# Kernel tuning notes

Measured on AMD Instinct MI355X. Metric: run time of the kernel, lower is better.

## Reference

```python
import jax, jax.numpy as jnp
import numpy as np

N_OBJECTS = 30
N_POINTS = 500
BATCH = 16384
ROT_WEIGHT = 1.0
TRANS_WEIGHT = 1.0


def quat_to_mat(q):
    # q: [B,4] (w,x,y,z) -> [B,3,3]; matches the module's (unnormalized) formula
    w, x, y, z = q[:, 0], q[:, 1], q[:, 2], q[:, 3]
    x2, y2, z2 = x * x, y * y, z * z
    xy, xz, yz = x * y, x * z, y * z
    wx, wy, wz = w * x, w * y, w * z
    row0 = jnp.stack([1 - 2 * y2 - 2 * z2, 2 * xy - 2 * wz, 2 * xz + 2 * wy], axis=1)
    row1 = jnp.stack([2 * xy + 2 * wz, 1 - 2 * x2 - 2 * z2, 2 * yz - 2 * wx], axis=1)
    row2 = jnp.stack([2 * xz - 2 * wy, 2 * yz + 2 * wx, 1 - 2 * x2 - 2 * y2], axis=1)
    return jnp.stack([row0, row1, row2], axis=1)


def setup_inputs() -> dict:
    key = jax.random.key(0)
    k1, k2, k3, k4, k5, k6 = jax.random.split(key, 6)
    pred_r = jax.random.normal(k1, (BATCH, 4), dtype=jnp.float32)
    pred_t = jax.random.normal(k2, (BATCH, 3), dtype=jnp.float32)
    gt_r = jax.random.normal(k3, (BATCH, 4), dtype=jnp.float32)
    gt_t = jax.random.normal(k4, (BATCH, 3), dtype=jnp.float32)
    obj_ids = jax.random.randint(k5, (BATCH,), 0, N_OBJECTS, dtype=jnp.int64)
    # sampled 3D model points per object (stand-in for loaded .ply meshes, in meters)
    points = jax.random.normal(k6, (N_OBJECTS, N_POINTS, 3), dtype=jnp.float32) * 0.1
    return {"pred_r": pred_r, "pred_t": pred_t, "gt_r": gt_r, "gt_t": gt_t,
            "obj_ids": obj_ids, "points": points}


def reference(pred_r, pred_t, gt_r, gt_t, obj_ids, points):
    Rp = quat_to_mat(pred_r)  # [B,3,3]
    Rg = quat_to_mat(gt_r)
    pts = points[obj_ids]  # [B,N,3] gather per-sample model points
    # pts @ R^T for both rotations; the difference is all that's needed for ADD/rot
    rot_diff = jnp.einsum('bij,bnj->bni', Rp - Rg, pts)  # [B,N,3]
    t_diff = pred_t - gt_t  # [B,3]
    add = jnp.linalg.norm(rot_diff + t_diff[:, None, :], axis=-1).mean(axis=1)  # [B]
    rot = jnp.linalg.norm(rot_diff, axis=-1).mean(axis=1)  # [B]
    trans = jnp.linalg.norm(t_diff, axis=-1)  # [B]
    return add.mean() + ROT_WEIGHT * rot.mean() + TRANS_WEIGHT * trans.mean()
```

## Files before the change

### kernel.cpp

```cpp
#include <hip/hip_runtime.h>

#define BATCH 16384
#define NPTS  500
#define NOBJ  30
#define EPW   2
#define WPB   4
#define NBLK  (BATCH / (EPW * WPB))

typedef float v2f __attribute__((ext_vector_type(2)));

__device__ __forceinline__ float fsqrt(float x) {
    return __builtin_amdgcn_sqrtf(x);
}

__global__ __launch_bounds__(256) void add_loss_stage1(
    const float* __restrict__ pred_r,
    const float* __restrict__ pred_t,
    const float* __restrict__ gt_r,
    const float* __restrict__ gt_t,
    const int*   __restrict__ obj_ids,
    const float* __restrict__ points,
    float* __restrict__ partial)
{
    const int wave  = threadIdx.x >> 6;
    const int lane  = threadIdx.x & 63;
    const int gwave = blockIdx.x * WPB + wave;
    const int b0    = gwave * EPW;

    float acc_pts   = 0.0f;
    float acc_trans = 0.0f;

    #pragma unroll
    for (int e = 0; e < EPW; ++e) {
        const int b = b0 + e;

        const float4 qp = ((const float4*)pred_r)[b];
        const float4 qg = ((const float4*)gt_r)[b];

        float pw=qp.x, px=qp.y, py=qp.z, pz=qp.w;
        float gw=qg.x, gx=qg.y, gy=qg.z, gz=qg.w;

        float d00 = 2.f*((gy*gy + gz*gz) - (py*py + pz*pz));
        float d01 = 2.f*((px*py - pw*pz) - (gx*gy - gw*gz));
        float d02 = 2.f*((px*pz + pw*py) - (gx*gz + gw*gy));
        float d10 = 2.f*((px*py + pw*pz) - (gx*gy + gw*gz));
        float d11 = 2.f*((gx*gx + gz*gz) - (px*px + pz*pz));
        float d12 = 2.f*((py*pz - pw*px) - (gy*gz - gw*gx));
        float d20 = 2.f*((px*pz - pw*py) - (gx*gz - gw*gy));
        float d21 = 2.f*((py*pz + pw*px) - (gy*gz + gw*gx));
        float d22 = 2.f*((gx*gx + gy*gy) - (px*px + py*py));

        float tdx = pred_t[3*b+0] - gt_t[3*b+0];
        float tdy = pred_t[3*b+1] - gt_t[3*b+1];
        float tdz = pred_t[3*b+2] - gt_t[3*b+2];

        const int obj = obj_ids[b];
        const float4* __restrict__ P4 = (const float4*)(points + (size_t)obj * (NPTS*3));

        float s = 0.0f;
        #pragma unroll
        for (int t = 0; t < 2; ++t) {
            const int g = t*64 + lane;
            if (t == 0 || lane < 61) {
                float4 a  = P4[3*g+0];
                float4 b4 = P4[3*g+1];
                float4 c  = P4[3*g+2];
                v2f xs[2] = { {a.x, a.w},  {b4.z, c.y} };
                v2f ys[2] = { {a.y, b4.x}, {b4.w, c.z} };
                v2f zs[2] = { {a.z, b4.y}, {c.x, c.w} };
                #pragma unroll
                for (int j = 0; j < 2; ++j) {
                    v2f x = xs[j], y = ys[j], z = zs[j];
                    v2f vx = d00*x + d01*y + d02*z;
                    v2f vy = d10*x + d11*y + d12*z;
                    v2f vz = d20*x + d21*y + d22*z;
                    v2f r  = vx*vx + vy*vy + vz*vz;
                    s += fsqrt(r.x) + fsqrt(r.y);
                    v2f ax = vx + tdx, ay = vy + tdy, az = vz + tdz;
                    v2f r2 = ax*ax + ay*ay + az*az;
                    s += fsqrt(r2.x) + fsqrt(r2.y);
                }
            }
        }

        acc_pts   += s;
        acc_trans += fsqrt(tdx*tdx + tdy*tdy + tdz*tdz);
    }

    #pragma unroll
    for (int off = 32; off > 0; off >>= 1)
        acc_pts += __shfl_down(acc_pts, off, 64);

    __shared__ float red[WPB];
    if (lane == 0)
        red[wave] = acc_pts * (1.0f / NPTS) + acc_trans;
    __syncthreads();
    if (threadIdx.x == 0)
        partial[blockIdx.x] = red[0] + red[1] + red[2] + red[3];
}

__global__ __launch_bounds__(256) void add_loss_stage2(
    const float* __restrict__ partial,
    float* __restrict__ out)
{
    const int wave = threadIdx.x >> 6;
    const int lane = threadIdx.x & 63;

    float s = 0.0f;
    #pragma unroll
    for (int k = 0; k < NBLK / 256; ++k)
        s += partial[k * 256 + threadIdx.x];

    #pragma unroll
    for (int off = 32; off > 0; off >>= 1)
        s += __shfl_down(s, off, 64);

    __shared__ float red[4];
    if (lane == 0) red[wave] = s;
    __syncthreads();
    if (threadIdx.x == 0)
        out[0] = (red[0] + red[1] + red[2] + red[3]) * (1.0f / BATCH);
}

extern "C" void kernel_launch(void* const* d_in, const int* in_sizes, int n_in,
                              void* d_out, int out_size, void* d_ws, size_t ws_size,
                              hipStream_t stream) {
    const float* pred_r  = (const float*)d_in[0];
    const float* pred_t  = (const float*)d_in[1];
    const float* gt_r    = (const float*)d_in[2];
    const float* gt_t    = (const float*)d_in[3];
    const int*   obj_ids = (const int*)d_in[4];
    const float* points  = (const float*)d_in[5];
    float* out     = (float*)d_out;
    float* partial = (float*)d_ws;

    add_loss_stage1<<<NBLK, 256, 0, stream>>>(
        pred_r, pred_t, gt_r, gt_t, obj_ids, points, partial);
    add_loss_stage2<<<1, 256, 0, stream>>>(partial, out);
}
```

Measured before the change: 72.69 us.

## Fuse two-stage reduction via last-block atomic counter and pack per-element setup

Replaces the separate second-stage reduction kernel with a last-block-done pattern. Each block stores its partial sum and bumps an atomic counter, and the final block reduces all partials and writes the output. The quaternion-to-matrix setup and translation loads for both elements are now done in packed two-wide vectors, and per-point sums go into a vector accumulator. This saves a kernel launch but adds a memset launch for the counter, plus atomic traffic and extra synchronization in every block.

Result: slower. 106.3 us (+46.2%).

```diff
diff --git a/kernel.cpp b/kernel.cpp
--- a/kernel.cpp
+++ b/kernel.cpp
@@ -13,51 +13,65 @@
     return __builtin_amdgcn_sqrtf(x);
 }
 
-__global__ __launch_bounds__(256) void add_loss_stage1(
+__global__ __launch_bounds__(256) void add_loss_fused(
     const float* __restrict__ pred_r,
     const float* __restrict__ pred_t,
     const float* __restrict__ gt_r,
     const float* __restrict__ gt_t,
     const int*   __restrict__ obj_ids,
     const float* __restrict__ points,
-    float* __restrict__ partial)
+    float* __restrict__ partial,
+    unsigned int* __restrict__ counter,
+    float* __restrict__ out)
 {
     const int wave  = threadIdx.x >> 6;
     const int lane  = threadIdx.x & 63;
     const int gwave = blockIdx.x * WPB + wave;
     const int b0    = gwave * EPW;
 
-    float acc_pts   = 0.0f;
-    float acc_trans = 0.0f;
+    const float4 qp0 = ((const float4*)pred_r)[b0 + 0];
+    const float4 qp1 = ((const float4*)pred_r)[b0 + 1];
+    const float4 qg0 = ((const float4*)gt_r)[b0 + 0];
+    const float4 qg1 = ((const float4*)gt_r)[b0 + 1];
+
+    v2f pw = {qp0.x, qp1.x}, px = {qp0.y, qp1.y}, py = {qp0.z, qp1.z}, pz = {qp0.w, qp1.w};
+    v2f gw = {qg0.x, qg1.x}, gx = {qg0.y, qg1.y}, gy = {qg0.z, qg1.z}, gz = {qg0.w, qg1.w};
+
+    v2f d00 = 2.f*((gy*gy + gz*gz) - (py*py + pz*pz));
+    v2f d01 = 2.f*((px*py - pw*pz) - (gx*gy - gw*gz));
+    v2f d02 = 2.f*((px*pz + pw*py) - (gx*gz + gw*gy));
+    v2f d10 = 2.f*((px*py + pw*pz) - (gx*gy + gw*gz));
+    v2f d11 = 2.f*((gx*gx + gz*gz) - (px*px + pz*pz));
+    v2f d12 = 2.f*((py*pz - pw*px) - (gy*gz - gw*gx));
+    v2f d20 = 2.f*((px*pz - pw*py) - (gx*gz - gw*gy));
+    v2f d21 = 2.f*((py*pz + pw*px) - (gy*gz + gw*gx));
+    v2f d22 = 2.f*((gx*gx + gy*gy) - (px*px + py*py));
+
+    const float2* PT2 = (const float2*)(pred_t + 3*b0);
+    const float2* GT2 = (const float2*)(gt_t  + 3*b0);
+    float2 ta = PT2[0], tb = PT2[1], tc = PT2[2];
+    float2 ua = GT2[0], ub = GT2[1], uc = GT2[2];
+    v2f tdx = { ta.x - ua.x, tb.y - ub.y };
+    v2f tdy = { ta.y - ua.y, tc.x - uc.x };
+    v2f tdz = { tb.x - ub.x, tc.y - uc.y };
+
+    v2f tq = tdx*tdx + tdy*tdy + tdz*tdz;
+    const float acc_trans = fsqrt(tq.x) + fsqrt(tq.y);
+
+    const int obj0 = obj_ids[b0 + 0];
+    const int obj1 = obj_ids[b0 + 1];
+
+    v2f sacc = {0.f, 0.f};
 
     #pragma unroll
     for (int e = 0; e < EPW; ++e) {
-        const int b = b0 + e;
-
-        const float4 qp = ((const float4*)pred_r)[b];
-        const float4 qg = ((const float4*)gt_r)[b];
-
-        float pw=qp.x, px=qp.y, py=qp.z, pz=qp.w;
-        float gw=qg.x, gx=qg.y, gy=qg.z, gz=qg.w;
-
-        float d00 = 2.f*((gy*gy + gz*gz) - (py*py + pz*pz));
-        float d01 = 2.f*((px*py - pw*pz) - (gx*gy - gw*gz));
-        float d02 = 2.f*((px*pz + pw*py) - (gx*gz + gw*gy));
-        float d10 = 2.f*((px*py + pw*pz) - (gx*gy + gw*gz));
-        float d11 = 2.f*((gx*gx + gz*gz) - (px*px + pz*pz));
-        float d12 = 2.f*((py*pz - pw*px) - (gy*gz - gw*gx));
-        float d20 = 2.f*((px*pz - pw*py) - (gx*gz - gw*gy));
-        float d21 = 2.f*((py*pz + pw*px) - (gy*gz + gw*gx));
-        float d22 = 2.f*((gx*gx + gy*gy) - (px*px + py*py));
-
-        float tdx = pred_t[3*b+0] - gt_t[3*b+0];
-        float tdy = pred_t[3*b+1] - gt_t[3*b+1];
-        float tdz = pred_t[3*b+2] - gt_t[3*b+2];
-
-        const int obj = obj_ids[b];
+        const float D00 = d00[e], D01 = d01[e], D02 = d02[e];
+        const float D10 = d10[e], D11 = d11[e], D12 = d12[e];
+        const float D20 = d20[e], D21 = d21[e], D22 = d22[e];
+        const float TX = tdx[e], TY = tdy[e], TZ = tdz[e];
+        const int obj = e ? obj1 : obj0;
         const float4* __restrict__ P4 = (const float4*)(points + (size_t)obj * (NPTS*3));
 
-        float s = 0.0f;
         #pragma unroll
         for (int t = 0; t < 2; ++t) {
             const int g = t*64 + lane;
@@ -71,22 +85,22 @@
                 #pragma unroll
                 for (int j = 0; j < 2; ++j) {
                     v2f x = xs[j], y = ys[j], z = zs[j];
-                    v2f vx = d00*x + d01*y + d02*z;
-                    v2f vy = d10*x + d11*y + d12*z;
-                    v2f vz = d20*x + d21*y + d22*z;
+                    v2f vx = D00*x + D01*y + D02*z;
+                    v2f vy = D10*x + D11*y + D12*z;
+                    v2f vz = D20*x + D21*y + D22*z;
                     v2f r  = vx*vx + vy*vy + vz*vz;
-                    s += fsqrt(r.x) + fsqrt(r.y);
-                    v2f ax = vx + tdx, ay = vy + tdy, az = vz + tdz;
+                    r.x = fsqrt(r.x); r.y = fsqrt(r.y);
+                    sacc += r;
+                    v2f ax = vx + TX, ay = vy + TY, az = vz + TZ;
                     v2f r2 = ax*ax + ay*ay + az*az;
-                    s += fsqrt(r2.x) + fsqrt(r2.y);
+                    r2.x = fsqrt(r2.x); r2.y = fsqrt(r2.y);
+                    sacc += r2;
                 }
             }
         }
-
-        acc_pts   += s;
-        acc_trans += fsqrt(tdx*tdx + tdy*tdy + tdz*tdz);
     }
 
+    float acc_pts = sacc.x + sacc.y;
     #pragma unroll
     for (int off = 32; off > 0; off >>= 1)
         acc_pts += __shfl_down(acc_pts, off, 64);
@@ -95,31 +109,33 @@
     if (lane == 0)
         red[wave] = acc_pts * (1.0f / NPTS) + acc_trans;
     __syncthreads();
-    if (threadIdx.x == 0)
-        partial[blockIdx.x] = red[0] + red[1] + red[2] + red[3];
-}
 
-__global__ __launch_bounds__(256) void add_loss_stage2(
-    const float* __restrict__ partial,
-    float* __restrict__ out)
-{
-    const int wave = threadIdx.x >> 6;
-    const int lane = threadIdx.x & 63;
+    __shared__ bool isLast;
+    if (threadIdx.x == 0) {
+        float bsum = red[0] + red[1] + red[2] + red[3];
+        __hip_atomic_store(&partial[blockIdx.x], bsum,
+                           __ATOMIC_RELAXED, __HIP_MEMORY_SCOPE_AGENT);
+        unsigned prev = __hip_atomic_fetch_add(counter, 1u,
+                           __ATOMIC_ACQ_REL, __HIP_MEMORY_SCOPE_AGENT);
+        isLast = (prev == NBLK - 1);
+    }
+    __syncthreads();
 
-    float s = 0.0f;
-    #pragma unroll
-    for (int k = 0; k < NBLK / 256; ++k)
-        s += partial[k * 256 + threadIdx.x];
-
-    #pragma unroll
-    for (int off = 32; off > 0; off >>= 1)
-        s += __shfl_down(s, off, 64);
-
-    __shared__ float red[4];
-    if (lane == 0) red[wave] = s;
-    __syncthreads();
-    if (threadIdx.x == 0)
-        out[0] = (red[0] + red[1] + red[2] + red[3]) * (1.0f / BATCH);
+    if (isLast) {
+        float s = 0.f;
+        #pragma unroll
+        for (int k = 0; k < NBLK / 256; ++k)
+            s += __hip_atomic_load(&partial[k*256 + (int)threadIdx.x],
+                                   __ATOMIC_RELAXED, __HIP_MEMORY_SCOPE_AGENT);
+        #pragma unroll
+        for (int off = 32; off > 0; off >>= 1)
+            s += __shfl_down(s, off, 64);
+        __shared__ float red2[WPB];
+        if (lane == 0) red2[wave] = s;
+        __syncthreads();
+        if (threadIdx.x == 0)
+            out[0] = (red2[0] + red2[1] + red2[2] + red2[3]) * (1.0f / BATCH);
+    }
 }
 
 extern "C" void kernel_launch(void* const* d_in, const int* in_sizes, int n_in,
@@ -133,8 +149,10 @@
     const float* points  = (const float*)d_in[5];
     float* out     = (float*)d_out;
     float* partial = (float*)d_ws;
+    unsigned int* counter = (unsigned int*)((char*)d_ws + NBLK * sizeof(float));
 
-    add_loss_stage1<<<NBLK, 256, 0, stream>>>(
-        pred_r, pred_t, gt_r, gt_t, obj_ids, points, partial);
-    add_loss_stage2<<<1, 256, 0, stream>>>(partial, out);
+    hipMemsetAsync(counter, 0, sizeof(unsigned int), stream);
+
+    add_loss_fused<<<NBLK, 256, 0, stream>>>(
+        pred_r, pred_t, gt_r, gt_t, obj_ids, points, partial, counter, out);
 }
```
